# Optimization experiments

Hardware: AMD Instinct MI355X
Metric: run time of the kernel (lower is better)

## Reference

```python
import jax, jax.numpy as jnp
import numpy as np

B, F, L = 16384, 32, 64
FEAT, DOM, R = 100000, 8, 16
D_IN = F * L  # 2048
N_HIDDEN = 3  # hidden_units = [256, 128, 1]


def _p(k, shape, scale=0.05):
    return jax.random.normal(k, shape, dtype=jnp.float32) * scale


def setup_inputs() -> dict:
    key = jax.random.key(0)
    ks = jax.random.split(key, 32)
    return {
        'x': jax.random.randint(ks[0], (B, F), 0, FEAT),
        'd': jax.random.randint(ks[1], (B,), 0, DOM),
        'emb': _p(ks[2], (FEAT, L)),
        # share MLP: 2048 -> 1024 -> 512 (ReLU after each)
        'sW0': _p(ks[3], (D_IN, 1024)), 'sb0': _p(ks[4], (1024,)),
        'sW1': _p(ks[5], (1024, 512)), 'sb1': _p(ks[6], (512,)),
        # domain layer: 512 -> 256 shared kernel + per-domain LoRA
        'Dk0': _p(ks[7], (512, 256)), 'Db0': _p(ks[8], (256,)),
        'DA0': _p(ks[9], (DOM, 512, R)), 'DB0': _p(ks[10], (DOM, R, 256)), 'Dlb0': _p(ks[11], (DOM, 256)),
        # task layers: 256 -> 128 -> 1 shared kernels + per-task LoRA
        'Tk0': _p(ks[12], (256, 128)), 'Tb0': _p(ks[13], (128,)),
        'Tk1': _p(ks[14], (128, 1)), 'Tb1': _p(ks[15], (1,)),
        'TA0': _p(ks[16], (2, 256, R)), 'TB0': _p(ks[17], (2, R, 128)), 'Tlb0': _p(ks[18], (2, 128)),
        'TA1': _p(ks[19], (2, 128, R)), 'TB1': _p(ks[20], (2, R, 1)), 'Tlb1': _p(ks[21], (2, 1)),
        # gate hypernet + heads
        'gW0': _p(ks[22], (D_IN, 1024)), 'gb0': _p(ks[23], (1024,)),
        'gW1': _p(ks[24], (1024, 512)), 'gb1': _p(ks[25], (512,)),
        'h0W': _p(ks[26], (512, 4)), 'h0b': _p(ks[27], (4,)),
        'h1W': _p(ks[28], (512, 4)), 'h1b': _p(ks[29], (4,)),
    }


def _mlp2(x, W0, b0, W1, b1):
    return jax.nn.relu(jax.nn.relu(x @ W0 + b0) @ W1 + b1)


def _forward(x, d, emb, sW0, sb0, sW1, sb1, Dk0, Db0, DA0, DB0, Dlb0,
             Tk0, Tb0, Tk1, Tb1, TA0, TB0, Tlb0, TA1, TB1, Tlb1,
             gW0, gb0, gW1, gb1, h0W, h0b, h1W, h1b):
    x_emb = emb[x].reshape(x.shape[0], -1)          # (B, dnn_dim)
    x_dnn = _mlp2(x_emb, sW0, sb0, sW1, sb1)        # (B, 512)

    # ---- domain layer (i=0), k=0 -> ReLU applied ----
    share = x_dnn @ Dk0 + Db0                        # (B, 256)
    lora = jnp.einsum('bi,bir->br', x_dnn, DA0[d])   # per-sample domain LoRA gather+matmul
    lora = jnp.einsum('br,bro->bo', lora, DB0[d]) + Dlb0[d]
    d_dnn = jax.nn.relu(share + lora)                # activated
    # d_share / d_lora kept PRE-activation, as in source

    t_dnn = [d_dnn, d_dnn]
    t_share = [share, share]
    t_lora = [lora, lora]
    t_sl, t_ls = [], []
    Tk, Tb = [Tk0, Tk1], [Tb0, Tb1]
    TA, TB, Tlb = [TA0, TA1], [TB0, TB1], [Tlb0, Tlb1]

    k = 1  # shared counter, faithfully incremented per (i, t) step
    for i in range(2):
        for t in range(2):
            ds = t_dnn[t] @ Tk[i] + Tb[i]
            ss = t_share[t] @ Tk[i] + Tb[i]
            ls = t_lora[t] @ Tk[i] + Tb[i]
            t_ls.append(ls)
            A, Bm, lb = TA[i][t], TB[i][t], Tlb[i][t]
            dl = (t_dnn[t] @ A) @ Bm + lb[None, :]
            sl = (t_share[t] @ A) @ Bm + lb[None, :]
            ll = (t_lora[t] @ A) @ Bm + lb[None, :]
            t_dnn[t] = ds + dl
            t_share[t] = ss
            t_lora[t] = ll
            t_sl.append(sl)
            if k + 1 < N_HIDDEN:  # only fires at (i=0, t=0)
                t_dnn[t] = jax.nn.relu(t_dnn[t])
                t_share[t] = jax.nn.relu(t_share[t])
                t_lora[t] = jax.nn.relu(t_lora[t])
                t_sl[t] = jax.nn.relu(t_sl[t])
                t_ls[t] = jax.nn.relu(t_ls[t])
                k += 1

    # ---- gating (hypernet sees detached embedding) ----
    hyper = _mlp2(jax.lax.stop_gradient(x_emb), gW0, gb0, gW1, gb1)
    gates = [jax.nn.sigmoid(hyper @ h0W + h0b), jax.nn.sigmoid(hyper @ h1W + h1b)]

    outs = []
    for t in range(2):
        g = gates[t]
        # t_dnn/t_share/t_lora are (B,1); t_sl[t]/t_ls[t] are (B,128) from i=0 -> broadcast (B,128)
        outs.append(t_dnn[t] - g[:, 0:1] * t_share[t] - g[:, 1:2] * t_lora[t]
                    - g[:, 2:3] * t_sl[t] - g[:, 3:4] * t_ls[t])
    return jnp.stack(outs)  # (2, B, 128)


def reference(x, d, emb, sW0, sb0, sW1, sb1, Dk0, Db0, DA0, DB0, Dlb0,
              Tk0, Tb0, Tk1, Tb1, TA0, TB0, Tlb0, TA1, TB1, Tlb1,
              gW0, gb0, gW1, gb1, h0W, h0b, h1W, h1b):
    return _forward(x, d, emb, sW0, sb0, sW1, sb1, Dk0, Db0, DA0, DB0, Dlb0,
                    Tk0, Tb0, Tk1, Tb1, TA0, TB0, Tlb0, TA1, TB1, Tlb1,
                    gW0, gb0, gW1, gb1, h0W, h0b, h1W, h1b)
```

## Files before the change

kernel.cpp:

```cpp
#include <hip/hip_runtime.h>
#include <hip/hip_bf16.h>

#define BATCH 16384

typedef __attribute__((ext_vector_type(4))) float f32x4;
typedef __attribute__((ext_vector_type(8))) short bf16x8;

__device__ inline float b2f(unsigned short u) {
    union { unsigned u; float f; } c; c.u = ((unsigned)u) << 16; return c.f;
}
__device__ inline unsigned short f2b(float f) {
    __hip_bfloat16 h = __float2bfloat16(f);
    return *(unsigned short*)&h;
}

#define GLL16(g, l)                                                            \
    __builtin_amdgcn_global_load_lds(                                          \
        (const __attribute__((address_space(1))) void*)(g),                    \
        (__attribute__((address_space(3))) void*)(l), 16, 0, 0)

__global__ void k_tcvt2(const float* __restrict__ src0, const float* __restrict__ src1,
                        int K, int N,
                        unsigned short* __restrict__ dst, int off0, int off1, int dst_ld)
{
    __shared__ float t[32][33];
    const float* src = blockIdx.z ? src1 : src0;
    int dst_off = blockIdx.z ? off1 : off0;
    int k0 = blockIdx.y * 32, n0 = blockIdx.x * 32;
    int tx = threadIdx.x, ty = threadIdx.y;
    #pragma unroll
    for (int s = 0; s < 32; s += 8) {
        int k = k0 + ty + s, n = n0 + tx;
        t[ty + s][tx] = (k < K && n < N) ? src[(size_t)k * N + n] : 0.f;
    }
    __syncthreads();
    #pragma unroll
    for (int s = 0; s < 32; s += 8) {
        int n = n0 + ty + s, k = k0 + tx;
        if (n < N && k < K)
            dst[(size_t)(dst_off + n) * dst_ld + k] = f2b(t[tx][ty + s]);
    }
}

__global__ __launch_bounds__(256) void k_smallprep(
    const float* __restrict__ sb0, const float* __restrict__ gb0,
    const float* __restrict__ sb1, const float* __restrict__ gb1,
    const float* __restrict__ Tb0,
    const float* __restrict__ DA0, const float* __restrict__ DB0,
    float* __restrict__ b1cat, float* __restrict__ b2cat, float* __restrict__ tb0c,
    unsigned short* __restrict__ DA0b, unsigned short* __restrict__ DB0b)
{
    int i = blockIdx.x * 256 + threadIdx.x;
    if (i < 1024)            { b1cat[i] = sb0[i]; return; }
    if (i < 2048)            { b1cat[i] = gb0[i - 1024]; return; }
    if (i < 2560)            { b2cat[i - 2048] = sb1[i - 2048]; return; }
    if (i < 3072)            { b2cat[i - 2560 + 512] = gb1[i - 2560]; return; }
    if (i < 3200)            { tb0c[i - 3072] = Tb0[i - 3072]; return; }
    if (i < 3232)            { tb0c[i - 3200 + 128] = 0.f; return; }
    i -= 3232;
    if (i < 65536)           { DA0b[i] = f2b(DA0[i]); return; }
    i -= 65536;
    if (i < 32768)           { DB0b[i] = f2b(DB0[i]); return; }
}

__global__ __launch_bounds__(256) void k_gather(const int* __restrict__ x,
                                                const float* __restrict__ emb,
                                                unsigned short* __restrict__ Xemb)
{
    int i = blockIdx.x * 256 + threadIdx.x;
    int b  = i >> 9;
    int j4 = (i & 511) << 2;
    int f  = j4 >> 6;
    int l  = j4 & 63;
    int idx = x[b * 32 + f];
    float4 v = *(const float4*)(emb + (size_t)idx * 64 + l);
    ushort4 o;
    o.x = f2b(v.x); o.y = f2b(v.y); o.z = f2b(v.z); o.w = f2b(v.w);
    *(ushort4*)(Xemb + (size_t)b * 2048 + j4) = o;
}

template<int RELU, int OUTBF16>
__global__ __launch_bounds__(512, 2) void k_gemm256(
    const unsigned short* __restrict__ A, int lda, long Az,
    const unsigned short* __restrict__ Bt, int K, long Bz,
    const float* __restrict__ bias, int biasz,
    void* __restrict__ C, int ldc, long Cz,
    int N)
{
    extern __shared__ char smem_raw[];
    const int NT = K >> 6;
    const int tid  = threadIdx.x;
    const int lane = tid & 63;
    const int w    = tid >> 6;
    const int wr   = w >> 2, wc = w & 3;
    const int frow = lane & 15, kg = lane >> 4;
    const int z = blockIdx.z;
    A    += (size_t)z * Az;
    Bt   += (size_t)z * Bz;
    bias += (size_t)z * biasz;

    const int gx  = gridDim.x;
    const int nwg = gx * gridDim.y;
    const int lin = blockIdx.y * gx + blockIdx.x;
    const int qq  = nwg >> 3;
    const int swz = (lin & 7) * qq + (lin >> 3);
    const int bx = swz % gx, by = swz / gx;
    const int row0 = by * 256, col0 = bx * 256;

    const int lch = (lane & 7) ^ ((lane >> 3) & 7);
    const unsigned short* gsrc[4];
    #pragma unroll
    for (int h = 0; h < 4; ++h) {
        int rr = h * 64 + w * 8 + (lane >> 3);
        if (lch < 4) gsrc[h] = A  + (size_t)(row0 + rr) * lda + lch * 8;
        else         gsrc[h] = Bt + (size_t)min(col0 + rr, N - 1) * K + (lch - 4) * 8;
    }
    const int dBase = w * 1024;

    const int pA = (kg ^ (frow & 7)) * 16;
    const int pB = ((4 + kg) ^ (frow & 7)) * 16;
    int aOff[8], bOff[4];
    #pragma unroll
    for (int m = 0; m < 8; ++m) aOff[m] = (wr * 128 + m * 16 + frow) * 128 + pA;
    #pragma unroll
    for (int n = 0; n < 4; ++n) bOff[n] = (wc * 64 + n * 16 + frow) * 128 + pB;

#define STAGE(t_, ks_, slot_) do {                                               \
        int s_ = min((int)(t_), NT - 1) * 64 + (ks_) * 32;                       \
        char* d_ = smem_raw + (slot_) * 65536 + (ks_) * 32768 + dBase;           \
        GLL16(gsrc[0] + s_, d_);                                                 \
        GLL16(gsrc[1] + s_, d_ + 8192);                                          \
        GLL16(gsrc[2] + s_, d_ + 16384);                                         \
        GLL16(gsrc[3] + s_, d_ + 24576);                                         \
    } while (0)
#define READS_B(sb_, ks_)                                                        \
        _Pragma("unroll")                                                        \
        for (int n = 0; n < 4; ++n)                                              \
            bfr[n] = *(const bf16x8*)(smem_raw + (sb_) + (ks_) * 32768 + bOff[n]);
#define READS_A(sb_, ks_, mh_)                                                   \
        _Pragma("unroll")                                                        \
        for (int mi = 0; mi < 4; ++mi)                                           \
            afr[mi] = *(const bf16x8*)(smem_raw + (sb_) + (ks_) * 32768 + aOff[(mh_) * 4 + mi]);
#define MFMA16(mh_) do {                                                         \
        __builtin_amdgcn_s_setprio(1);                                           \
        _Pragma("unroll")                                                        \
        for (int mi = 0; mi < 4; ++mi)                                           \
            _Pragma("unroll")                                                    \
            for (int n = 0; n < 4; ++n)                                          \
                acc[(mh_) * 4 + mi][n] = __builtin_amdgcn_mfma_f32_16x16x32_bf16( \
                    bfr[n], afr[mi], acc[(mh_) * 4 + mi][n], 0, 0, 0);           \
        __builtin_amdgcn_s_setprio(0);                                           \
    } while (0)
#define LGKM0 asm volatile("s_waitcnt lgkmcnt(0)" ::: "memory")
#define VM4   asm volatile("s_waitcnt vmcnt(4)" ::: "memory")
#define BAR   __builtin_amdgcn_s_barrier()

    f32x4 acc[8][4] = {};
    bf16x8 afr[4], bfr[4];

    STAGE(0, 0, 0); STAGE(0, 1, 0);
    VM4; BAR;

    for (int t = 0; t < NT; ++t) {
        const int slot = t & 1, nslot = slot ^ 1;
        const int sb = slot * 65536;
        READS_B(sb, 0); READS_A(sb, 0, 0);
        STAGE(t + 1, 0, nslot);
        BAR; LGKM0; MFMA16(0); BAR;
        READS_A(sb, 0, 1);
        VM4;
        BAR; LGKM0; MFMA16(1); BAR;
        READS_B(sb, 1); READS_A(sb, 1, 0);
        STAGE(t + 1, 1, nslot);
        BAR; LGKM0; MFMA16(0); BAR;
        READS_A(sb, 1, 1);
        VM4;
        BAR; LGKM0; MFMA16(1); BAR;
    }
#undef STAGE
#undef READS_B
#undef READS_A
#undef MFMA16
#undef LGKM0
#undef VM4
#undef BAR

    #pragma unroll
    for (int m = 0; m < 8; ++m) {
        int row = row0 + wr * 128 + m * 16 + frow;
        #pragma unroll
        for (int n = 0; n < 4; ++n) {
            int col = col0 + wc * 64 + n * 16 + kg * 4;
            float4 bv = *(const float4*)(bias + col);
            float v0 = acc[m][n][0] + bv.x, v1 = acc[m][n][1] + bv.y;
            float v2 = acc[m][n][2] + bv.z, v3 = acc[m][n][3] + bv.w;
            if (RELU) {
                v0 = fmaxf(v0, 0.f); v1 = fmaxf(v1, 0.f);
                v2 = fmaxf(v2, 0.f); v3 = fmaxf(v3, 0.f);
            }
            if (OUTBF16) {
                ushort4 o = { f2b(v0), f2b(v1), f2b(v2), f2b(v3) };
                *(ushort4*)((unsigned short*)C + (size_t)z * Cz + (size_t)row * ldc + col) = o;
            } else {
                float4 o = { v0, v1, v2, v3 };
                *(float4*)((float*)C + (size_t)z * Cz + (size_t)row * ldc + col) = o;
            }
        }
    }
}

template<int RELU, int OUTBF16>
__global__ __launch_bounds__(256) void k_gemm(
    const unsigned short* __restrict__ A, int lda,
    const unsigned short* __restrict__ Bt,
    const float* __restrict__ bias,
    void* __restrict__ C, int ldc,
    int N, int K)
{
    __shared__ __align__(16) unsigned short As[128 * 32];
    __shared__ __align__(16) unsigned short Bs[128 * 32];
    const int tid  = threadIdx.x;
    const int lane = tid & 63;
    const int w    = tid >> 6;
    const int wr   = w >> 1, wc = w & 1;
    const int row0 = blockIdx.y * 128;
    const int col0 = blockIdx.x * 128;
    const int frow = lane & 15;
    const int kg   = lane >> 4;
    const int sw   = kg ^ ((frow >> 1) & 3);

    const int srow = w * 32 + (lane >> 2);
    const int csw  = (lane & 3) ^ ((lane >> 3) & 3);
    const int br0  = min(col0 + srow, N - 1);
    const int br1  = min(col0 + srow + 16, N - 1);

    const unsigned short* a0 = A  + (size_t)(row0 + srow) * lda      + csw * 8;
    const unsigned short* a1 = A  + (size_t)(row0 + srow + 16) * lda + csw * 8;
    const unsigned short* b0 = Bt + (size_t)br0 * K + csw * 8;
    const unsigned short* b1 = Bt + (size_t)br1 * K + csw * 8;
    unsigned short* lA0 = As + (w * 2 + 0) * 512;
    unsigned short* lA1 = As + (w * 2 + 1) * 512;
    unsigned short* lB0 = Bs + (w * 2 + 0) * 512;
    unsigned short* lB1 = Bs + (w * 2 + 1) * 512;

    f32x4 acc[4][4] = {};

    for (int bk = 0; bk < K; bk += 32) {
        __syncthreads();
        GLL16(a0 + bk, lA0);
        GLL16(a1 + bk, lA1);
        GLL16(b0 + bk, lB0);
        GLL16(b1 + bk, lB1);
        __syncthreads();
        bf16x8 af[4], bfr[4];
        #pragma unroll
        for (int m = 0; m < 4; ++m)
            af[m] = *(const bf16x8*)&As[(wr * 64 + m * 16 + frow) * 32 + sw * 8];
        #pragma unroll
        for (int n = 0; n < 4; ++n)
            bfr[n] = *(const bf16x8*)&Bs[(wc * 64 + n * 16 + frow) * 32 + sw * 8];
        #pragma unroll
        for (int m = 0; m < 4; ++m)
            #pragma unroll
            for (int n = 0; n < 4; ++n)
                acc[m][n] = __builtin_amdgcn_mfma_f32_16x16x32_bf16(bfr[n], af[m], acc[m][n], 0, 0, 0);
    }

    #pragma unroll
    for (int m = 0; m < 4; ++m) {
        int row = row0 + wr * 64 + m * 16 + frow;
        #pragma unroll
        for (int n = 0; n < 4; ++n) {
            int col = col0 + wc * 64 + n * 16 + kg * 4;
            if (col >= N) continue;
            float4 bv = *(const float4*)(bias + col);
            float v0 = acc[m][n][0] + bv.x, v1 = acc[m][n][1] + bv.y;
            float v2 = acc[m][n][2] + bv.z, v3 = acc[m][n][3] + bv.w;
            if (RELU) {
                v0 = fmaxf(v0, 0.f); v1 = fmaxf(v1, 0.f);
                v2 = fmaxf(v2, 0.f); v3 = fmaxf(v3, 0.f);
            }
            if (OUTBF16) {
                ushort4 o = { f2b(v0), f2b(v1), f2b(v2), f2b(v3) };
                *(ushort4*)((unsigned short*)C + (size_t)row * ldc + col) = o;
            } else {
                float4 o = { v0, v1, v2, v3 };
                *(float4*)((float*)C + (size_t)row * ldc + col) = o;
            }
        }
    }
}

__global__ __launch_bounds__(256) void k_dlora(
    const unsigned short* __restrict__ Xdnn, const int* __restrict__ d,
    const unsigned short* __restrict__ DA0b, const unsigned short* __restrict__ DB0b,
    const float* __restrict__ Dlb0,
    const unsigned short* __restrict__ SHARE,
    unsigned short* __restrict__ LORA, unsigned short* __restrict__ DDNN)
{
    int w = threadIdx.x >> 6, lane = threadIdx.x & 63;
    int b = blockIdx.x * 4 + w;
    int dom = d[b];
    uint4 raw = *(const uint4*)(Xdnn + (size_t)b * 512 + lane * 8);
    const unsigned short* pr = (const unsigned short*)&raw;
    float xv[8];
    #pragma unroll
    for (int j = 0; j < 8; ++j) xv[j] = b2f(pr[j]);

    const unsigned short* Ap = DA0b + ((size_t)dom * 512 + lane * 8) * 16;
    float v[16];
    #pragma unroll
    for (int r = 0; r < 16; ++r) v[r] = 0.f;
    #pragma unroll
    for (int j = 0; j < 8; ++j) {
        uint4 a0 = *(const uint4*)(Ap + j * 16);
        uint4 a1 = *(const uint4*)(Ap + j * 16 + 8);
        const unsigned short* ap = (const unsigned short*)&a0;
        const unsigned short* aq = (const unsigned short*)&a1;
        float xj = xv[j];
        #pragma unroll
        for (int r = 0; r < 8; ++r) v[r]     += xj * b2f(ap[r]);
        #pragma unroll
        for (int r = 0; r < 8; ++r) v[r + 8] += xj * b2f(aq[r]);
    }
    #pragma unroll
    for (int s = 1; s < 64; s <<= 1) {
        #pragma unroll
        for (int r = 0; r < 16; ++r) v[r] += __shfl_xor(v[r], s, 64);
    }
    const unsigned short* Bp = DB0b + (size_t)dom * 16 * 256;
    const float* lbp = Dlb0 + (size_t)dom * 256;
    #pragma unroll
    for (int c = 0; c < 4; ++c) {
        int o = lane + c * 64;
        float a = lbp[o];
        #pragma unroll
        for (int r = 0; r < 16; ++r) a += v[r] * b2f(Bp[r * 256 + o]);
        float sh = b2f(SHARE[(size_t)b * 256 + o]);
        LORA[(size_t)b * 256 + o] = f2b(a);
        DDNN[(size_t)b * 256 + o] = f2b(fmaxf(sh + a, 0.f));
    }
}

__global__ __launch_bounds__(256) void k_tail(
    const float* __restrict__ Yd, const float* __restrict__ Ys, const float* __restrict__ Yl,
    const unsigned short* __restrict__ Hyper,
    const float* __restrict__ TB0, const float* __restrict__ Tlb0,
    const float* __restrict__ Tk1, const float* __restrict__ Tb1,
    const float* __restrict__ TA1, const float* __restrict__ TB1, const float* __restrict__ Tlb1,
    const float* __restrict__ h0W, const float* __restrict__ h0b,
    const float* __restrict__ h1W, const float* __restrict__ h1b,
    float* __restrict__ out)
{
    __shared__ float sTB0[2][16][128];
    __shared__ float sTlb0[2][128];
    __shared__ float sTk1[128];
    __shared__ float sWeff[2][128];
    __shared__ float sY[4][3][160];
    const int tid = threadIdx.x;

    for (int i = tid; i < 4096; i += 256) ((float*)sTB0)[i] = TB0[i];
    if (tid < 256) ((float*)sTlb0)[tid] = Tlb0[tid];
    if (tid < 128) sTk1[tid] = Tk1[tid];
    {
        int t = tid >> 7, j = tid & 127;
        float a = 0.f;
        #pragma unroll
        for (int r = 0; r < 16; ++r) a += TA1[((size_t)t * 128 + j) * 16 + r] * TB1[t * 16 + r];
        sWeff[t][j] = a;
    }
    const float* Yp[3] = {Yd, Ys, Yl};
    int b0 = blockIdx.x * 4;
    for (int i = tid; i < 4 * 3 * 160; i += 256) {
        int s = i / 480, rem = i % 480, st = rem / 160, idx = rem % 160;
        sY[s][st][idx] = Yp[st][(size_t)(b0 + s) * 160 + idx];
    }
    __syncthreads();

    int w = tid >> 6, lane = tid & 63;
    int b = b0 + w;
    const float* yd = sY[w][0];
    const float* ys = sY[w][1];
    const float* yl = sY[w][2];
    int j0 = lane, j1 = lane + 64;

    uint4 hraw = *(const uint4*)(Hyper + (size_t)b * 512 + lane * 8);
    const unsigned short* hp = (const unsigned short*)&hraw;
    float hv[8];
    #pragma unroll
    for (int j = 0; j < 8; ++j) hv[j] = b2f(hp[j]);

    float red[14];
    #pragma unroll
    for (int k = 0; k < 14; ++k) red[k] = 0.f;
    #pragma unroll
    for (int j = 0; j < 8; ++j) {
        float4 w0 = *(const float4*)(h0W + (size_t)(lane * 8 + j) * 4);
        float4 w1 = *(const float4*)(h1W + (size_t)(lane * 8 + j) * 4);
        red[0] += hv[j] * w0.x; red[1] += hv[j] * w0.y; red[2] += hv[j] * w0.z; red[3] += hv[j] * w0.w;
        red[4] += hv[j] * w1.x; red[5] += hv[j] * w1.y; red[6] += hv[j] * w1.z; red[7] += hv[j] * w1.w;
    }

    float SLv[2][2], LSv[2][2];
    #pragma unroll
    for (int t = 0; t < 2; ++t) {
        float lb0 = sTlb0[t][j0], lb1 = sTlb0[t][j1];
        float dl0 = lb0, dl1 = lb1, sl0 = lb0, sl1 = lb1, ll0 = lb0, ll1 = lb1;
        #pragma unroll
        for (int r = 0; r < 16; ++r) {
            float w0v = sTB0[t][r][j0], w1v = sTB0[t][r][j1];
            float ud = yd[128 + t * 16 + r];
            float us = ys[128 + t * 16 + r];
            float ul = yl[128 + t * 16 + r];
            dl0 += ud * w0v; dl1 += ud * w1v;
            sl0 += us * w0v; sl1 += us * w1v;
            ll0 += ul * w0v; ll1 += ul * w1v;
        }
        float D0 = yd[j0] + dl0, D1 = yd[j1] + dl1;
        float S0 = ys[j0],       S1 = ys[j1];
        float L0 = ll0,          L1 = ll1;
        float sl_0 = sl0, sl_1 = sl1;
        float ls_0 = yl[j0], ls_1 = yl[j1];
        if (t == 0) {
            D0 = fmaxf(D0, 0.f); D1 = fmaxf(D1, 0.f);
            S0 = fmaxf(S0, 0.f); S1 = fmaxf(S1, 0.f);
            L0 = fmaxf(L0, 0.f); L1 = fmaxf(L1, 0.f);
            sl_0 = fmaxf(sl_0, 0.f); sl_1 = fmaxf(sl_1, 0.f);
            ls_0 = fmaxf(ls_0, 0.f); ls_1 = fmaxf(ls_1, 0.f);
        }
        SLv[t][0] = sl_0; SLv[t][1] = sl_1;
        LSv[t][0] = ls_0; LSv[t][1] = ls_1;
        float we0 = sWeff[t][j0], we1 = sWeff[t][j1];
        float tk0 = sTk1[j0],     tk1v = sTk1[j1];
        red[8 + t * 3 + 0] = D0 * (tk0 + we0) + D1 * (tk1v + we1);
        red[8 + t * 3 + 1] = S0 * tk0 + S1 * tk1v;
        red[8 + t * 3 + 2] = L0 * we0 + L1 * we1;
    }

    #pragma unroll
    for (int s = 1; s < 64; s <<= 1) {
        #pragma unroll
        for (int k = 0; k < 14; ++k) red[k] += __shfl_xor(red[k], s, 64);
    }

    float Tb1v = Tb1[0];
    #pragma unroll
    for (int t = 0; t < 2; ++t) {
        float fd = red[8 + t * 3 + 0] + Tb1v + Tlb1[t];
        float fs = red[8 + t * 3 + 1] + Tb1v;
        float fl = red[8 + t * 3 + 2] + Tlb1[t];
        const float* hb = t ? h1b : h0b;
        float g0 = 1.f / (1.f + expf(-(red[t * 4 + 0] + hb[0])));
        float g1 = 1.f / (1.f + expf(-(red[t * 4 + 1] + hb[1])));
        float g2 = 1.f / (1.f + expf(-(red[t * 4 + 2] + hb[2])));
        float g3 = 1.f / (1.f + expf(-(red[t * 4 + 3] + hb[3])));
        float base = fd - g0 * fs - g1 * fl;
        size_t o = (size_t)t * BATCH * 128 + (size_t)b * 128;
        out[o + j0] = base - g2 * SLv[t][0] - g3 * LSv[t][0];
        out[o + j1] = base - g2 * SLv[t][1] - g3 * LSv[t][1];
    }
}

extern "C" void kernel_launch(void* const* d_in, const int* in_sizes, int n_in,
                              void* d_out, int out_size, void* d_ws, size_t ws_size,
                              hipStream_t stream)
{
    const int*   x    = (const int*)  d_in[0];
    const int*   dix  = (const int*)  d_in[1];
    const float* emb  = (const float*)d_in[2];
    const float* sW0  = (const float*)d_in[3];
    const float* sb0  = (const float*)d_in[4];
    const float* sW1  = (const float*)d_in[5];
    const float* sb1  = (const float*)d_in[6];
    const float* Dk0  = (const float*)d_in[7];
    const float* Db0  = (const float*)d_in[8];
    const float* DA0  = (const float*)d_in[9];
    const float* DB0  = (const float*)d_in[10];
    const float* Dlb0 = (const float*)d_in[11];
    const float* Tk0  = (const float*)d_in[12];
    const float* Tb0  = (const float*)d_in[13];
    const float* Tk1  = (const float*)d_in[14];
    const float* Tb1  = (const float*)d_in[15];
    const float* TA0  = (const float*)d_in[16];
    const float* TB0  = (const float*)d_in[17];
    const float* Tlb0 = (const float*)d_in[18];
    const float* TA1  = (const float*)d_in[19];
    const float* TB1  = (const float*)d_in[20];
    const float* Tlb1 = (const float*)d_in[21];
    const float* gW0  = (const float*)d_in[22];
    const float* gb0  = (const float*)d_in[23];
    const float* gW1  = (const float*)d_in[24];
    const float* gb1  = (const float*)d_in[25];
    const float* h0W  = (const float*)d_in[26];
    const float* h0b  = (const float*)d_in[27];
    const float* h1W  = (const float*)d_in[28];
    const float* h1b  = (const float*)d_in[29];

    hipFuncSetAttribute((const void*)k_gemm256<1, 1>,
                        hipFuncAttributeMaxDynamicSharedMemorySize, 131072);

    char* ws = (char*)d_ws;
    size_t off = 0;
    auto alloc = [&](size_t bytes) -> void* {
        void* p = ws + off;
        off += (bytes + 255) & ~(size_t)255;
        return p;
    };
    unsigned short* W1t   = (unsigned short*)alloc((size_t)2048 * 2048 * 2);
    unsigned short* W2cat = (unsigned short*)alloc((size_t)1024 * 1024 * 2);
    unsigned short* Dk0t  = (unsigned short*)alloc((size_t)256 * 512 * 2);
    unsigned short* Tcat  = (unsigned short*)alloc((size_t)160 * 256 * 2);
    unsigned short* DA0b  = (unsigned short*)alloc((size_t)8 * 512 * 16 * 2);
    unsigned short* DB0b  = (unsigned short*)alloc((size_t)8 * 16 * 256 * 2);
    float*          b1cat = (float*)alloc(2048 * 4);
    float*          b2cat = (float*)alloc(1024 * 4);
    float*          tb0c  = (float*)alloc(160 * 4);
    char* regA = (char*)alloc((size_t)BATCH * 2048 * 2);
    char* regB = (char*)alloc((size_t)BATCH * 2048 * 2);
    unsigned short* Xdnn  = (unsigned short*)alloc((size_t)BATCH * 512 * 2);
    unsigned short* Hyper = (unsigned short*)alloc((size_t)BATCH * 512 * 2);

    unsigned short* Xemb = (unsigned short*)regA;
    float* Ybase = (float*)regA;
    float* Ys = Ybase;
    float* Yl = Ybase + (size_t)BATCH * 160;
    float* Yd = Ybase + (size_t)2 * BATCH * 160;
    unsigned short* Hbuf  = (unsigned short*)regB;
    unsigned short* SHARE = (unsigned short*)regB;
    unsigned short* LORA  = SHARE + (size_t)BATCH * 256;
    unsigned short* DDNN  = LORA  + (size_t)BATCH * 256;

    dim3 tb(32, 8);
    k_tcvt2<<<dim3(32, 64, 2), tb, 0, stream>>>(sW0, gW0, 2048, 1024, W1t, 0, 1024, 2048);
    k_tcvt2<<<dim3(16, 32, 2), tb, 0, stream>>>(sW1, gW1, 1024, 512, W2cat, 0, 512, 1024);
    k_tcvt2<<<dim3(8, 16, 1),  tb, 0, stream>>>(Dk0, Dk0, 512, 256, Dk0t, 0, 0, 512);
    k_tcvt2<<<dim3(4, 8, 1),   tb, 0, stream>>>(Tk0, Tk0, 256, 128, Tcat, 0, 0, 256);
    k_tcvt2<<<dim3(1, 8, 2),   tb, 0, stream>>>(TA0, TA0 + 256 * 16, 256, 16, Tcat, 128, 144, 256);
    k_smallprep<<<397, 256, 0, stream>>>(sb0, gb0, sb1, gb1, Tb0, DA0, DB0,
                                         b1cat, b2cat, tb0c, DA0b, DB0b);

    k_gather<<<32768, 256, 0, stream>>>(x, emb, Xemb);
    k_gemm256<1, 1><<<dim3(8, 64, 1), 512, 131072, stream>>>(
        Xemb, 2048, 0, W1t, 2048, 0, b1cat, 0, Hbuf, 2048, 0, 2048);
    k_gemm256<1, 1><<<dim3(2, 64, 2), 512, 131072, stream>>>(
        Hbuf, 2048, 1024, W2cat, 1024, (long)512 * 1024, b2cat, 512,
        Xdnn, 512, (long)BATCH * 512, 512);
    k_gemm<0, 1><<<dim3(2, 128), 256, 0, stream>>>(Xdnn, 512, Dk0t, Db0, SHARE, 256, 256, 512);
    k_dlora<<<BATCH / 4, 256, 0, stream>>>(Xdnn, dix, DA0b, DB0b, Dlb0, SHARE, LORA, DDNN);
    k_gemm<0, 0><<<dim3(2, 384), 256, 0, stream>>>(SHARE, 256, Tcat, tb0c, Ybase, 160, 160, 256);
    k_tail<<<BATCH / 4, 256, 0, stream>>>(Yd, Ys, Yl, Hyper, TB0, Tlb0, Tk1, Tb1,
                                          TA1, TB1, Tlb1, h0W, h0b, h1W, h1b, (float*)d_out);
}
```

Measured before the change: 378.7 us.

## Halve GEMM LDS stage depth and simplify the double-buffered K pipeline

The main 256x256 bf16 GEMM now stages 32-wide K slices instead of 64-wide ones. This halves dynamic LDS to 64KB and cuts the barrier/waitcnt sequence per iteration, prefetching two slices ahead into alternating slots. Launch bounds are raised to request 4 blocks per CU, aiming for more resident blocks to hide latency. The tighter occupancy target may force heavy register spilling of the 128-float accumulator, and each iteration does less MFMA work per barrier.

Measured after the change: 1.507 ms. +297.8%, slower.

```diff
diff --git a/kernel.cpp b/kernel.cpp
--- a/kernel.cpp
+++ b/kernel.cpp
@@ -80,7 +80,7 @@
 }
 
 template<int RELU, int OUTBF16>
-__global__ __launch_bounds__(512, 2) void k_gemm256(
+__global__ __launch_bounds__(512, 4) void k_gemm256(
     const unsigned short* __restrict__ A, int lda, long Az,
     const unsigned short* __restrict__ Bt, int K, long Bz,
     const float* __restrict__ bias, int biasz,
@@ -88,7 +88,7 @@
     int N)
 {
     extern __shared__ char smem_raw[];
-    const int NT = K >> 6;
+    const int NS = K >> 5;
     const int tid  = threadIdx.x;
     const int lane = tid & 63;
     const int w    = tid >> 6;
@@ -125,22 +125,22 @@
     #pragma unroll
     for (int n = 0; n < 4; ++n) bOff[n] = (wc * 64 + n * 16 + frow) * 128 + pB;
 
-#define STAGE(t_, ks_, slot_) do {                                               \
-        int s_ = min((int)(t_), NT - 1) * 64 + (ks_) * 32;                       \
-        char* d_ = smem_raw + (slot_) * 65536 + (ks_) * 32768 + dBase;           \
+#define STAGE(sIdx, slot_) do {                                                  \
+        int s_ = min((int)(sIdx), NS - 1) * 32;                                  \
+        char* d_ = smem_raw + (slot_) * 32768 + dBase;                           \
         GLL16(gsrc[0] + s_, d_);                                                 \
         GLL16(gsrc[1] + s_, d_ + 8192);                                          \
         GLL16(gsrc[2] + s_, d_ + 16384);                                         \
         GLL16(gsrc[3] + s_, d_ + 24576);                                         \
     } while (0)
-#define READS_B(sb_, ks_)                                                        \
+#define READS_B(sb_)                                                             \
         _Pragma("unroll")                                                        \
         for (int n = 0; n < 4; ++n)                                              \
-            bfr[n] = *(const bf16x8*)(smem_raw + (sb_) + (ks_) * 32768 + bOff[n]);
-#define READS_A(sb_, ks_, mh_)                                                   \
+            bfr[n] = *(const bf16x8*)(smem_raw + (sb_) + bOff[n]);
+#define READS_A(sb_, mh_)                                                        \
         _Pragma("unroll")                                                        \
         for (int mi = 0; mi < 4; ++mi)                                           \
-            afr[mi] = *(const bf16x8*)(smem_raw + (sb_) + (ks_) * 32768 + aOff[(mh_) * 4 + mi]);
+            afr[mi] = *(const bf16x8*)(smem_raw + (sb_) + aOff[(mh_) * 4 + mi]);
 #define MFMA16(mh_) do {                                                         \
         __builtin_amdgcn_s_setprio(1);                                           \
         _Pragma("unroll")                                                        \
@@ -151,39 +151,31 @@
                     bfr[n], afr[mi], acc[(mh_) * 4 + mi][n], 0, 0, 0);           \
         __builtin_amdgcn_s_setprio(0);                                           \
     } while (0)
-#define LGKM0 asm volatile("s_waitcnt lgkmcnt(0)" ::: "memory")
-#define VM4   asm volatile("s_waitcnt vmcnt(4)" ::: "memory")
-#define BAR   __builtin_amdgcn_s_barrier()
 
     f32x4 acc[8][4] = {};
     bf16x8 afr[4], bfr[4];
 
-    STAGE(0, 0, 0); STAGE(0, 1, 0);
-    VM4; BAR;
-
-    for (int t = 0; t < NT; ++t) {
-        const int slot = t & 1, nslot = slot ^ 1;
-        const int sb = slot * 65536;
-        READS_B(sb, 0); READS_A(sb, 0, 0);
-        STAGE(t + 1, 0, nslot);
-        BAR; LGKM0; MFMA16(0); BAR;
-        READS_A(sb, 0, 1);
-        VM4;
-        BAR; LGKM0; MFMA16(1); BAR;
-        READS_B(sb, 1); READS_A(sb, 1, 0);
-        STAGE(t + 1, 1, nslot);
-        BAR; LGKM0; MFMA16(0); BAR;
-        READS_A(sb, 1, 1);
-        VM4;
-        BAR; LGKM0; MFMA16(1); BAR;
+    STAGE(0, 0); STAGE(1, 1);
+    asm volatile("s_waitcnt vmcnt(4)" ::: "memory");
+    __builtin_amdgcn_s_barrier();
+
+    for (int t = 0; t < NS; ++t) {
+        const int slot = t & 1;
+        const int sb = slot * 32768;
+        READS_B(sb); READS_A(sb, 0);
+        MFMA16(0);
+        READS_A(sb, 1);
+        asm volatile("s_waitcnt lgkmcnt(0)" ::: "memory");
+        __builtin_amdgcn_s_barrier();
+        STAGE(t + 2, slot);
+        MFMA16(1);
+        asm volatile("s_waitcnt vmcnt(4)" ::: "memory");
+        __builtin_amdgcn_s_barrier();
     }
 #undef STAGE
 #undef READS_B
 #undef READS_A
 #undef MFMA16
-#undef LGKM0
-#undef VM4
-#undef BAR
 
     #pragma unroll
     for (int m = 0; m < 8; ++m) {
@@ -497,7 +489,7 @@
     const float* h1b  = (const float*)d_in[29];
 
     hipFuncSetAttribute((const void*)k_gemm256<1, 1>,
-                        hipFuncAttributeMaxDynamicSharedMemorySize, 131072);
+                        hipFuncAttributeMaxDynamicSharedMemorySize, 65536);
 
     char* ws = (char*)d_ws;
     size_t off = 0;
@@ -540,9 +532,9 @@
                                          b1cat, b2cat, tb0c, DA0b, DB0b);
 
     k_gather<<<32768, 256, 0, stream>>>(x, emb, Xemb);
-    k_gemm256<1, 1><<<dim3(8, 64, 1), 512, 131072, stream>>>(
+    k_gemm256<1, 1><<<dim3(8, 64, 1), 512, 65536, stream>>>(
         Xemb, 2048, 0, W1t, 2048, 0, b1cat, 0, Hbuf, 2048, 0, 2048);
-    k_gemm256<1, 1><<<dim3(2, 64, 2), 512, 131072, stream>>>(
+    k_gemm256<1, 1><<<dim3(2, 64, 2), 512, 65536, stream>>>(
         Hbuf, 2048, 1024, W2cat, 1024, (long)512 * 1024, b2cat, 512,
         Xdnn, 512, (long)BATCH * 512, 512);
     k_gemm<0, 1><<<dim3(2, 128), 256, 0, stream>>>(Xdnn, 512, Dk0t, Db0, SHARE, 256, 256, 512);
```

## Fuse embedding gather into first GEMM and merge prep kernels into one launch

Applied to the files above, without the earlier changes.

The separate gather kernel that materialised a bf16 embedding matrix (B x 2048) is removed. Instead the whole embedding table is converted to bf16 once in a merged prep kernel, and the first GEMM loads its A tiles straight from the table using per-row indices staged in LDS. All the weight transpose and convert launches are folded into one kernel with a single grid. This drops a 64MB write and re-read of Xemb plus several launches, but it converts the full 100k-row table every call and raises the GEMM's LDS to 160KB, which may affect occupancy.

New measurement: 354.0 us. 6.5% less time.

```diff
diff --git a/kernel.cpp b/kernel.cpp
--- a/kernel.cpp
+++ b/kernel.cpp
@@ -19,73 +19,86 @@
         (const __attribute__((address_space(1))) void*)(g),                    \
         (__attribute__((address_space(3))) void*)(l), 16, 0, 0)
 
-__global__ void k_tcvt2(const float* __restrict__ src0, const float* __restrict__ src1,
-                        int K, int N,
-                        unsigned short* __restrict__ dst, int off0, int off1, int dst_ld)
-{
-    __shared__ float t[32][33];
-    const float* src = blockIdx.z ? src1 : src0;
-    int dst_off = blockIdx.z ? off1 : off0;
-    int k0 = blockIdx.y * 32, n0 = blockIdx.x * 32;
-    int tx = threadIdx.x, ty = threadIdx.y;
-    #pragma unroll
-    for (int s = 0; s < 32; s += 8) {
-        int k = k0 + ty + s, n = n0 + tx;
-        t[ty + s][tx] = (k < K && n < N) ? src[(size_t)k * N + n] : 0.f;
-    }
-    __syncthreads();
-    #pragma unroll
-    for (int s = 0; s < 32; s += 8) {
-        int n = n0 + ty + s, k = k0 + tx;
-        if (n < N && k < K)
-            dst[(size_t)(dst_off + n) * dst_ld + k] = f2b(t[tx][ty + s]);
-    }
-}
-
-__global__ __launch_bounds__(256) void k_smallprep(
+__global__ __launch_bounds__(256) void k_prep(
+    const float* __restrict__ sW0, const float* __restrict__ gW0,
+    const float* __restrict__ sW1, const float* __restrict__ gW1,
+    const float* __restrict__ Dk0, const float* __restrict__ Tk0,
+    const float* __restrict__ TA0,
     const float* __restrict__ sb0, const float* __restrict__ gb0,
     const float* __restrict__ sb1, const float* __restrict__ gb1,
-    const float* __restrict__ Tb0,
-    const float* __restrict__ DA0, const float* __restrict__ DB0,
+    const float* __restrict__ Tb0, const float* __restrict__ DA0,
+    const float* __restrict__ DB0, const float* __restrict__ emb,
+    unsigned short* __restrict__ W1t, unsigned short* __restrict__ W2cat,
+    unsigned short* __restrict__ Dk0t, unsigned short* __restrict__ Tcat,
     float* __restrict__ b1cat, float* __restrict__ b2cat, float* __restrict__ tb0c,
-    unsigned short* __restrict__ DA0b, unsigned short* __restrict__ DB0b)
+    unsigned short* __restrict__ DA0b, unsigned short* __restrict__ DB0b,
+    unsigned short* __restrict__ embB)
 {
-    int i = blockIdx.x * 256 + threadIdx.x;
-    if (i < 1024)            { b1cat[i] = sb0[i]; return; }
-    if (i < 2048)            { b1cat[i] = gb0[i - 1024]; return; }
-    if (i < 2560)            { b2cat[i - 2048] = sb1[i - 2048]; return; }
-    if (i < 3072)            { b2cat[i - 2560 + 512] = gb1[i - 2560]; return; }
-    if (i < 3200)            { tb0c[i - 3072] = Tb0[i - 3072]; return; }
-    if (i < 3232)            { tb0c[i - 3200 + 128] = 0.f; return; }
-    i -= 3232;
-    if (i < 65536)           { DA0b[i] = f2b(DA0[i]); return; }
-    i -= 65536;
-    if (i < 32768)           { DB0b[i] = f2b(DB0[i]); return; }
-}
-
-__global__ __launch_bounds__(256) void k_gather(const int* __restrict__ x,
-                                                const float* __restrict__ emb,
-                                                unsigned short* __restrict__ Xemb)
-{
-    int i = blockIdx.x * 256 + threadIdx.x;
-    int b  = i >> 9;
-    int j4 = (i & 511) << 2;
-    int f  = j4 >> 6;
-    int l  = j4 & 63;
-    int idx = x[b * 32 + f];
-    float4 v = *(const float4*)(emb + (size_t)idx * 64 + l);
-    ushort4 o;
-    o.x = f2b(v.x); o.y = f2b(v.y); o.z = f2b(v.z); o.w = f2b(v.w);
-    *(ushort4*)(Xemb + (size_t)b * 2048 + j4) = o;
-}
-
-template<int RELU, int OUTBF16>
+    int id = blockIdx.x;
+    const int tid = threadIdx.x;
+    __shared__ float t[32][33];
+    auto tcvt = [&](const float* src, int K, int N, unsigned short* dst,
+                    int dst_off, int dst_ld, int bx, int by) {
+        int k0 = by * 32, n0 = bx * 32;
+        int tx = tid & 31, ty = tid >> 5;
+        #pragma unroll
+        for (int s = 0; s < 32; s += 8) {
+            int k = k0 + ty + s, n = n0 + tx;
+            t[ty + s][tx] = (k < K && n < N) ? src[(size_t)k * N + n] : 0.f;
+        }
+        __syncthreads();
+        #pragma unroll
+        for (int s = 0; s < 32; s += 8) {
+            int n = n0 + ty + s, k = k0 + tx;
+            if (n < N && k < K)
+                dst[(size_t)(dst_off + n) * dst_ld + k] = f2b(t[tx][ty + s]);
+        }
+    };
+    if (id < 4096) { int z = id >> 11, rem = id & 2047;
+        tcvt(z ? gW0 : sW0, 2048, 1024, W1t, z * 1024, 2048, rem & 31, rem >> 5); return; }
+    id -= 4096;
+    if (id < 1024) { int z = id >> 9, rem = id & 511;
+        tcvt(z ? gW1 : sW1, 1024, 512, W2cat, z * 512, 1024, rem & 15, rem >> 4); return; }
+    id -= 1024;
+    if (id < 128) { tcvt(Dk0, 512, 256, Dk0t, 0, 512, id & 7, id >> 3); return; }
+    id -= 128;
+    if (id < 32)  { tcvt(Tk0, 256, 128, Tcat, 0, 256, id & 3, id >> 2); return; }
+    id -= 32;
+    if (id < 16)  { int z = id >> 3;
+        tcvt(TA0 + z * 256 * 16, 256, 16, Tcat, 128 + z * 16, 256, 0, id & 7); return; }
+    id -= 16;
+    if (id < 397) {
+        int i = id * 256 + tid;
+        if (i < 1024)            { b1cat[i] = sb0[i]; return; }
+        if (i < 2048)            { b1cat[i] = gb0[i - 1024]; return; }
+        if (i < 2560)            { b2cat[i - 2048] = sb1[i - 2048]; return; }
+        if (i < 3072)            { b2cat[i - 2560 + 512] = gb1[i - 2560]; return; }
+        if (i < 3200)            { tb0c[i - 3072] = Tb0[i - 3072]; return; }
+        if (i < 3232)            { tb0c[i - 3200 + 128] = 0.f; return; }
+        i -= 3232;
+        if (i < 65536)           { DA0b[i] = f2b(DA0[i]); return; }
+        i -= 65536;
+        if (i < 32768)           { DB0b[i] = f2b(DB0[i]); return; }
+        return;
+    }
+    id -= 397;
+    {
+        int e = (id * 256 + tid) * 4;
+        if (e < 100000 * 64) {
+            float4 v = *(const float4*)(emb + e);
+            ushort4 o = { f2b(v.x), f2b(v.y), f2b(v.z), f2b(v.w) };
+            *(ushort4*)(embB + e) = o;
+        }
+    }
+}
+
+template<int RELU, int OUTBF16, int GATHER>
 __global__ __launch_bounds__(512, 2) void k_gemm256(
     const unsigned short* __restrict__ A, int lda, long Az,
     const unsigned short* __restrict__ Bt, int K, long Bz,
     const float* __restrict__ bias, int biasz,
     void* __restrict__ C, int ldc, long Cz,
-    int N)
+    int N, const int* __restrict__ xsrc, const unsigned short* __restrict__ embB)
 {
     extern __shared__ char smem_raw[];
     const int NT = K >> 6;
@@ -108,12 +121,17 @@
     const int row0 = by * 256, col0 = bx * 256;
 
     const int lch = (lane & 7) ^ ((lane >> 3) & 7);
+    const int isA = (lch < 4);
+    const int eoBase = lch * 8;
+    const int* xb = (const int*)(smem_raw + 131072);
+    int rrh[4];
     const unsigned short* gsrc[4];
     #pragma unroll
     for (int h = 0; h < 4; ++h) {
         int rr = h * 64 + w * 8 + (lane >> 3);
-        if (lch < 4) gsrc[h] = A  + (size_t)(row0 + rr) * lda + lch * 8;
-        else         gsrc[h] = Bt + (size_t)min(col0 + rr, N - 1) * K + (lch - 4) * 8;
+        rrh[h] = rr;
+        if (isA) gsrc[h] = GATHER ? embB : A + (size_t)(row0 + rr) * lda + lch * 8;
+        else     gsrc[h] = Bt + (size_t)min(col0 + rr, N - 1) * K + (lch - 4) * 8;
     }
     const int dBase = w * 1024;
 
@@ -126,12 +144,25 @@
     for (int n = 0; n < 4; ++n) bOff[n] = (wc * 64 + n * 16 + frow) * 128 + pB;
 
 #define STAGE(t_, ks_, slot_) do {                                               \
-        int s_ = min((int)(t_), NT - 1) * 64 + (ks_) * 32;                       \
+        int tc_ = min((int)(t_), NT - 1);                                        \
         char* d_ = smem_raw + (slot_) * 65536 + (ks_) * 32768 + dBase;           \
-        GLL16(gsrc[0] + s_, d_);                                                 \
-        GLL16(gsrc[1] + s_, d_ + 8192);                                          \
-        GLL16(gsrc[2] + s_, d_ + 16384);                                         \
-        GLL16(gsrc[3] + s_, d_ + 24576);                                         \
+        if (GATHER) {                                                            \
+            _Pragma("unroll")                                                    \
+            for (int h_ = 0; h_ < 4; ++h_) {                                     \
+                int ix_ = xb[rrh[h_] * 32 + tc_];                                \
+                const unsigned short* sa_ = embB + (size_t)ix_ * 64              \
+                                            + (ks_) * 32 + eoBase;               \
+                const unsigned short* sb_ = gsrc[h_] + tc_ * 64 + (ks_) * 32;    \
+                const unsigned short* s_  = isA ? sa_ : sb_;                     \
+                GLL16(s_, d_ + h_ * 8192);                                       \
+            }                                                                    \
+        } else {                                                                 \
+            int o_ = tc_ * 64 + (ks_) * 32;                                      \
+            GLL16(gsrc[0] + o_, d_);                                             \
+            GLL16(gsrc[1] + o_, d_ + 8192);                                      \
+            GLL16(gsrc[2] + o_, d_ + 16384);                                     \
+            GLL16(gsrc[3] + o_, d_ + 24576);                                     \
+        }                                                                        \
     } while (0)
 #define READS_B(sb_, ks_)                                                        \
         _Pragma("unroll")                                                        \
@@ -158,6 +189,15 @@
     f32x4 acc[8][4] = {};
     bf16x8 afr[4], bfr[4];
 
+    if (GATHER) {
+        const char* xs = (const char*)(xsrc + row0 * 32);
+        #pragma unroll
+        for (int r = 0; r < 4; ++r)
+            GLL16(xs + r * 8192 + w * 1024 + lane * 16,
+                  smem_raw + 131072 + r * 8192 + w * 1024);
+        asm volatile("s_waitcnt vmcnt(0)" ::: "memory");
+        __builtin_amdgcn_s_barrier();
+    }
     STAGE(0, 0, 0); STAGE(0, 1, 0);
     VM4; BAR;
 
@@ -496,7 +536,9 @@
     const float* h1W  = (const float*)d_in[28];
     const float* h1b  = (const float*)d_in[29];
 
-    hipFuncSetAttribute((const void*)k_gemm256<1, 1>,
+    hipFuncSetAttribute((const void*)k_gemm256<1, 1, 1>,
+                        hipFuncAttributeMaxDynamicSharedMemorySize, 163840);
+    hipFuncSetAttribute((const void*)k_gemm256<1, 1, 0>,
                         hipFuncAttributeMaxDynamicSharedMemorySize, 131072);
 
     char* ws = (char*)d_ws;
@@ -512,16 +554,15 @@
     unsigned short* Tcat  = (unsigned short*)alloc((size_t)160 * 256 * 2);
     unsigned short* DA0b  = (unsigned short*)alloc((size_t)8 * 512 * 16 * 2);
     unsigned short* DB0b  = (unsigned short*)alloc((size_t)8 * 16 * 256 * 2);
+    unsigned short* embB  = (unsigned short*)alloc((size_t)100000 * 64 * 2);
     float*          b1cat = (float*)alloc(2048 * 4);
     float*          b2cat = (float*)alloc(1024 * 4);
     float*          tb0c  = (float*)alloc(160 * 4);
-    char* regA = (char*)alloc((size_t)BATCH * 2048 * 2);
+    float*          Ybase = (float*)alloc((size_t)3 * BATCH * 160 * 4);
     char* regB = (char*)alloc((size_t)BATCH * 2048 * 2);
     unsigned short* Xdnn  = (unsigned short*)alloc((size_t)BATCH * 512 * 2);
     unsigned short* Hyper = (unsigned short*)alloc((size_t)BATCH * 512 * 2);
 
-    unsigned short* Xemb = (unsigned short*)regA;
-    float* Ybase = (float*)regA;
     float* Ys = Ybase;
     float* Yl = Ybase + (size_t)BATCH * 160;
     float* Yd = Ybase + (size_t)2 * BATCH * 160;
@@ -530,21 +571,16 @@
     unsigned short* LORA  = SHARE + (size_t)BATCH * 256;
     unsigned short* DDNN  = LORA  + (size_t)BATCH * 256;
 
-    dim3 tb(32, 8);
-    k_tcvt2<<<dim3(32, 64, 2), tb, 0, stream>>>(sW0, gW0, 2048, 1024, W1t, 0, 1024, 2048);
-    k_tcvt2<<<dim3(16, 32, 2), tb, 0, stream>>>(sW1, gW1, 1024, 512, W2cat, 0, 512, 1024);
-    k_tcvt2<<<dim3(8, 16, 1),  tb, 0, stream>>>(Dk0, Dk0, 512, 256, Dk0t, 0, 0, 512);
-    k_tcvt2<<<dim3(4, 8, 1),   tb, 0, stream>>>(Tk0, Tk0, 256, 128, Tcat, 0, 0, 256);
-    k_tcvt2<<<dim3(1, 8, 2),   tb, 0, stream>>>(TA0, TA0 + 256 * 16, 256, 16, Tcat, 128, 144, 256);
-    k_smallprep<<<397, 256, 0, stream>>>(sb0, gb0, sb1, gb1, Tb0, DA0, DB0,
-                                         b1cat, b2cat, tb0c, DA0b, DB0b);
-
-    k_gather<<<32768, 256, 0, stream>>>(x, emb, Xemb);
-    k_gemm256<1, 1><<<dim3(8, 64, 1), 512, 131072, stream>>>(
-        Xemb, 2048, 0, W1t, 2048, 0, b1cat, 0, Hbuf, 2048, 0, 2048);
-    k_gemm256<1, 1><<<dim3(2, 64, 2), 512, 131072, stream>>>(
+    k_prep<<<11943, 256, 0, stream>>>(
+        sW0, gW0, sW1, gW1, Dk0, Tk0, TA0,
+        sb0, gb0, sb1, gb1, Tb0, DA0, DB0, emb,
+        W1t, W2cat, Dk0t, Tcat, b1cat, b2cat, tb0c, DA0b, DB0b, embB);
+
+    k_gemm256<1, 1, 1><<<dim3(8, 64, 1), 512, 163840, stream>>>(
+        embB, 0, 0, W1t, 2048, 0, b1cat, 0, Hbuf, 2048, 0, 2048, x, embB);
+    k_gemm256<1, 1, 0><<<dim3(2, 64, 2), 512, 131072, stream>>>(
         Hbuf, 2048, 1024, W2cat, 1024, (long)512 * 1024, b2cat, 512,
-        Xdnn, 512, (long)BATCH * 512, 512);
+        Xdnn, 512, (long)BATCH * 512, 512, nullptr, nullptr);
     k_gemm<0, 1><<<dim3(2, 128), 256, 0, stream>>>(Xdnn, 512, Dk0t, Db0, SHARE, 256, 256, 512);
     k_dlora<<<BATCH / 4, 256, 0, stream>>>(Xdnn, dix, DA0b, DB0b, Dlb0, SHARE, LORA, DDNN);
     k_gemm<0, 0><<<dim3(2, 384), 256, 0, stream>>>(SHARE, 256, Tcat, tb0c, Ybase, 160, 160, 256);
```
